# Kernel optimization log

Hardware: AMD Instinct MI355X
Metric: run time of the kernel (lower is better)

Reference implementation:

```python
import jax, jax.numpy as jnp
import numpy as np

B, L, E = 256, 8192, 64
PS_HIGH, PS_LOW = 3, 12
THR = 1.5
WINDOW = 9
K = 5
MAXP = (L + PS_HIGH - 1) // PS_HIGH  # max possible patches per row


def setup_inputs() -> dict:
    key = jax.random.key(0)
    k1, k2, k3, k4, k5 = jax.random.split(key, 5)
    x = jax.random.randint(k1, (B, L), 0, K)  # int tokens in [0, K)
    w1 = jax.random.normal(k2, (E, 1), jnp.float32)        # Linear(1, E) weight
    b1 = jax.random.normal(k3, (E,), jnp.float32) * 0.1
    w2 = jax.random.normal(k4, (E, E), jnp.float32) / np.float32(np.sqrt(E))  # Linear(E, E) weight
    b2 = jax.random.normal(k5, (E,), jnp.float32) * 0.1
    return {"x": x, "w1": w1, "b1": b1, "w2": w2, "b2": b2}


def calc_entropy(x):
    # one-hot counts in a sliding window of size WINDOW (same as conv1d with ones kernel, groups=K)
    oh = jax.nn.one_hot(jnp.clip(x, 0, K - 1), K, dtype=jnp.float32)  # [B, L, K]
    oh = jnp.moveaxis(oh, -1, 1)                                       # [B, K, L]
    pad = WINDOW // 2
    padded = jnp.pad(oh, ((0, 0), (0, 0), (pad, pad)))                 # [B, K, L+2*pad]
    cs = jnp.cumsum(padded, axis=-1)
    csz = jnp.pad(cs, ((0, 0), (0, 0), (1, 0)))
    counts = csz[..., WINDOW:] - csz[..., :-WINDOW]                    # [B, K, L]
    total = jnp.clip(counts.sum(axis=1, keepdims=True), 1e-12, None)
    probs = counts / total
    entropy = -(probs * jnp.log2(probs + 1e-12)).sum(axis=1)           # [B, L]
    return entropy


def seg_row(cs_row, ent_row):
    # cs_row: [L+1] prefix sums of x (float); ent_row: [L] entropy
    def step(i, _):
        ent_i = ent_row[jnp.minimum(i, L - 1)]
        psize = jnp.where(ent_i > THR, PS_HIGH, PS_LOW).astype(jnp.int32)
        j = jnp.minimum(i + psize, L)
        valid = i < L
        mean = (cs_row[j] - cs_row[i]) / jnp.maximum(j - i, 1).astype(jnp.float32)
        return j, (mean, valid)

    _, (means, valids) = jax.lax.scan(step, jnp.int32(0), None, length=MAXP)
    return means, valids  # [MAXP], [MAXP]


def reference(x, w1, b1, w2, b2):
    entropy = calc_entropy(x)
    # prefix sums for O(1) per-patch means
    cs = jnp.pad(jnp.cumsum(x.astype(jnp.float32), axis=1), ((0, 0), (1, 0)))  # [B, L+1]
    means, valids = jax.vmap(seg_row)(cs, entropy)  # [B, MAXP], [B, MAXP]
    # batched tiny MLP over all candidate patches: Linear(1,E) -> ReLU -> Linear(E,E)
    h = jax.nn.relu(means[..., None] * w1[:, 0] + b1)  # [B, MAXP, E]
    vec = h @ w2.T + b2                                # [B, MAXP, E]
    m = valids[..., None].astype(jnp.float32)
    blt_features = (vec * m).sum(axis=1) / m.sum(axis=1)  # [B, E]
    return blt_features, entropy
```

## Files before the change

### kernel.cpp

```cpp
#include <hip/hip_runtime.h>
#include <math.h>


constexpr int B_ = 256;
constexpr int L_ = 8192;
constexpr int E_ = 64;
constexpr int T_ = 1024;
constexpr int PT = 8;
constexpr int CHUNK = 128;
constexpr int NCH = L_ / CHUNK;
constexpr int MAXPC = 44;

__global__ __launch_bounds__(1024)
void entropy_patcher_kernel(const int* __restrict__ x,
                            const float* __restrict__ w1,
                            const float* __restrict__ b1,
                            const float* __restrict__ w2,
                            const float* __restrict__ b2,
                            float* __restrict__ dout) {
  __shared__ __align__(16) unsigned char tok8p[8 + L_ + 8];
  __shared__ __align__(16) float csBuf[L_ + 4];
  __shared__ __align__(16) float meanbuf[NCH][MAXPC];
  __shared__ __align__(16) float tripleTab[1000];
  __shared__ __align__(16) unsigned char maskBytes[T_];
  __shared__ unsigned char exitT[NCH][12];
  __shared__ float rcpTab[13];
  __shared__ float hTab[10];
  __shared__ float l2Tab[13];
  __shared__ int cntC[NCH];
  __shared__ int waveTot[16];
  __shared__ float Sred[16][E_];
  __shared__ float partG[16][E_];
  __shared__ float avgv[E_];
  __shared__ int PcountS;

  const int tid  = threadIdx.x;
  const int lane = tid & 63;
  const int wv   = tid >> 6;
  const int b    = blockIdx.x;

  const int* xr = x + b * L_;
  float* entOut = dout + (size_t)B_ * E_ + (size_t)b * L_;

  const int4 v0 = ((const int4*)xr)[2 * tid];
  const int4 v1 = ((const int4*)xr)[2 * tid + 1];
  unsigned pw0 = (unsigned)v0.x | ((unsigned)v0.y << 8) |
                 ((unsigned)v0.z << 16) | ((unsigned)v0.w << 24);
  unsigned pw1 = (unsigned)v1.x | ((unsigned)v1.y << 8) |
                 ((unsigned)v1.z << 16) | ((unsigned)v1.w << 24);
  *(uint2*)(tok8p + 8 + 8 * tid) = make_uint2(pw0, pw1);
  if (tid == 0) *(uint2*)(tok8p) = make_uint2(~0u, ~0u);
  if (tid == 1) *(uint2*)(tok8p + 8 + L_) = make_uint2(~0u, ~0u);
  if (tid < 1000) {
    int a = tid / 100;
    int r = tid - 100 * a;
    int bq = r / 10, cq = r - 10 * bq;
    float pa = (float)a / 9.0f, pb = (float)bq / 9.0f, pc = (float)cq / 9.0f;
    float fa = -(pa * log2f(pa + 1e-12f));
    float fb = -(pb * log2f(pb + 1e-12f));
    float fc = -(pc * log2f(pc + 1e-12f));
    tripleTab[tid] = fa + fb + fc;
  }
  if (tid >= 1000 && tid < 1010) {
    int n = tid - 1000;
    hTab[n] = (n > 0) ? (float)n * log2f((float)n) : 0.0f;
  }
  if (tid >= 1000 && tid < 1013) {
    int n = tid - 1000;
    rcpTab[n] = 1.0f / (float)(n == 0 ? 1 : n);
  }
  if (tid >= 1010 && tid < 1023) {
    int n = tid - 1010;
    l2Tab[n] = (n > 0) ? log2f((float)n) : 0.0f;
  }
  __syncthreads();

  unsigned long long tw0 = *(const unsigned long long*)(tok8p + 8 * tid);
  unsigned long long tw1 = *(const unsigned long long*)(tok8p + 8 * tid + 8);
  unsigned long long tw2 = *(const unsigned long long*)(tok8p + 8 * tid + 16);
  unsigned code[20];
  #pragma unroll
  for (int l = 4; l < 20; ++l) {
    unsigned byte = (l < 8)  ? (unsigned)((tw0 >> (8 * l)) & 0xff)
                  : (l < 16) ? (unsigned)((tw1 >> (8 * (l - 8))) & 0xff)
                             : (unsigned)((tw2 >> (8 * (l - 16))) & 0xff);
    code[l] = (byte <= 4u) ? (1u << (6 * byte)) : 0u;
  }
  unsigned s = 0;
  #pragma unroll
  for (int l = 4; l <= 12; ++l) s += code[l];
  float entv[PT];
  #pragma unroll
  for (int q = 0; q < PT; ++q) {
    if (q) s += code[q + 12] - code[q + 3];
    unsigned a  = s & 63u,        bb = (s >> 6) & 63u, cc = (s >> 12) & 63u;
    unsigned dd = (s >> 18) & 63u, ee = (s >> 24) & 63u;
    unsigned i1 = a * 100u + bb * 10u + cc;
    unsigned i2 = dd * 100u + ee * 10u;
    entv[q] = tripleTab[i1] + tripleTab[i2];
  }
  if (tid == 0 || tid == T_ - 1) {
    #pragma unroll
    for (int q = 0; q < PT; ++q) {
      int p = 8 * tid + q;
      if (p < 4 || p >= L_ - 4) {
        unsigned ss = 0;
        for (int l = q + 4; l <= q + 12; ++l) ss += code[l];
        unsigned cn[5] = { ss & 63u, (ss >> 6) & 63u, (ss >> 12) & 63u,
                           (ss >> 18) & 63u, (ss >> 24) & 63u };
        int tsum = (int)(cn[0] + cn[1] + cn[2] + cn[3] + cn[4]);
        float sh = hTab[cn[0]] + hTab[cn[1]] + hTab[cn[2]] + hTab[cn[3]] + hTab[cn[4]];
        entv[q] = l2Tab[tsum] - rcpTab[tsum] * sh;
      }
    }
  }
  ((float4*)entOut)[2 * tid]     = make_float4(entv[0], entv[1], entv[2], entv[3]);
  ((float4*)entOut)[2 * tid + 1] = make_float4(entv[4], entv[5], entv[6], entv[7]);
  unsigned mbyte = 0;
  #pragma unroll
  for (int q = 0; q < PT; ++q) mbyte |= (entv[q] > 1.5f ? 1u : 0u) << q;
  maskBytes[tid] = (unsigned char)mbyte;

  int tk[8];
  #pragma unroll
  for (int j = 0; j < 4; ++j) {
    tk[j]     = (int)((pw0 >> (8 * j)) & 0xffu);
    tk[4 + j] = (int)((pw1 >> (8 * j)) & 0xffu);
  }
  int ls = tk[0] + tk[1] + tk[2] + tk[3] + tk[4] + tk[5] + tk[6] + tk[7];
  int incl = ls;
  #pragma unroll
  for (int d = 1; d < 64; d <<= 1) {
    int up = __shfl_up(incl, d, 64);
    if (lane >= d) incl += up;
  }
  if (lane == 63) waveTot[wv] = incl;
  __syncthreads();
  int base = 0;
  #pragma unroll
  for (int q = 0; q < 16; ++q) base += (q < wv) ? waveTot[q] : 0;
  float acc = (float)(base + incl - ls);
  {
    float4 c0, c1;
    c0.x = acc; acc += (float)tk[0]; c0.y = acc; acc += (float)tk[1];
    c0.z = acc; acc += (float)tk[2]; c0.w = acc; acc += (float)tk[3];
    c1.x = acc; acc += (float)tk[4]; c1.y = acc; acc += (float)tk[5];
    c1.z = acc; acc += (float)tk[6]; c1.w = acc; acc += (float)tk[7];
    ((float4*)csBuf)[2 * tid] = c0; ((float4*)csBuf)[2 * tid + 1] = c1;
    if (tid == T_ - 1) csBuf[L_] = acc;
  }

  unsigned long long m0 = 0, m1 = 0;
  if (tid < 768) {
    int c = tid & 63, o = tid >> 6;
    m0 = *(const unsigned long long*)(maskBytes + 16 * c);
    m1 = *(const unsigned long long*)(maskBytes + 16 * c + 8);
    int p = o;
    while (p < CHUNK) {
      unsigned long long mm = (p & 64) ? m1 : m0;
      p += ((mm >> (p & 63)) & 1ULL) ? 3 : 12;
    }
    exitT[c][o] = (unsigned char)(p - CHUNK);
  }
  __syncthreads();

  int myOff = 0;
  if (tid < 64) {
    const unsigned* ep = (const unsigned*)&exitT[tid][0];
    unsigned u0 = ep[0], u1 = ep[1], u2 = ep[2];
    auto nib = [](unsigned w) {
      return (w & 0xFu) | ((w >> 4) & 0xF0u) | ((w >> 8) & 0xF00u) | ((w >> 12) & 0xF000u);
    };
    unsigned long long tab = (unsigned long long)nib(u0)
                           | ((unsigned long long)nib(u1) << 16)
                           | ((unsigned long long)nib(u2) << 32);
    #pragma unroll
    for (int d = 1; d < 64; d <<= 1) {
      unsigned long long other =
          (unsigned long long)__shfl_up((long long)tab, d, 64);
      if (lane >= d) {
        unsigned long long nt = 0;
        #pragma unroll
        for (int e = 0; e < 12; ++e) {
          unsigned oe  = (unsigned)((other >> (4 * e)) & 15ULL);
          unsigned val = (unsigned)((tab >> (4 * oe)) & 15ULL);
          nt |= (unsigned long long)val << (4 * e);
        }
        tab = nt;
      }
    }
    unsigned long long prev = (unsigned long long)__shfl_up((long long)tab, 1, 64);
    myOff = (lane == 0) ? 0 : (int)(prev & 15ULL);

    int c = tid;
    int p = CHUNK * c + myOff;
    const int end = CHUNK * c + CHUNK;
    float csp = csBuf[p];
    int n = 0;
    while (p < end) {
      int lp = p - CHUNK * c;
      unsigned long long mm = (lp & 64) ? m1 : m0;
      int ps = ((mm >> (lp & 63)) & 1ULL) ? 3 : 12;
      int j = p + ps; if (j > L_) j = L_;
      float csj = csBuf[j];
      meanbuf[c][n++] = (csj - csp) * rcpTab[j - p];
      csp = csj; p = j;
    }
    cntC[c] = n;
    int tot = n;
    #pragma unroll
    for (int d2 = 32; d2; d2 >>= 1) tot += __shfl_xor(tot, d2, 64);
    if (lane == 0) PcountS = tot;
  }
  __syncthreads();

  {
    const float w1v = w1[lane];
    const float b1v = b1[lane];
    float S = 0.0f;
    for (int c = wv; c < NCH; c += 16) {
      int n = cntC[c];
      const float* mb = &meanbuf[c][0];
      int j = 0;
      for (; j + 4 <= n; j += 4) {
        float4 m4 = *((const float4*)(mb + j));
        S += fmaxf(fmaf(m4.x, w1v, b1v), 0.0f);
        S += fmaxf(fmaf(m4.y, w1v, b1v), 0.0f);
        S += fmaxf(fmaf(m4.z, w1v, b1v), 0.0f);
        S += fmaxf(fmaf(m4.w, w1v, b1v), 0.0f);
      }
      for (; j < n; ++j) S += fmaxf(fmaf(mb[j], w1v, b1v), 0.0f);
    }
    Sred[wv][lane] = S;
  }
  __syncthreads();
  if (tid < 64) {
    float sm = 0.f;
    #pragma unroll
    for (int q = 0; q < 16; ++q) sm += Sred[q][tid];
    avgv[tid] = sm / (float)PcountS;
  }
  __syncthreads();

  {
    float acc2 = 0.f;
    #pragma unroll
    for (int kk = 0; kk < 4; ++kk) {
      int k = 4 * wv + kk;
      acc2 = fmaf(avgv[k], w2[lane * 64 + k], acc2);
    }
    partG[wv][lane] = acc2;
  }
  __syncthreads();
  if (tid < 64) {
    float r = b2[tid];
    #pragma unroll
    for (int q = 0; q < 16; ++q) r += partG[q][tid];
    dout[(size_t)b * E_ + tid] = r;
  }
}

extern "C" void kernel_launch(void* const* d_in, const int* in_sizes, int n_in,
                              void* d_out, int out_size, void* d_ws, size_t ws_size,
                              hipStream_t stream) {
  const int*   x  = (const int*)d_in[0];
  const float* w1 = (const float*)d_in[1];
  const float* b1 = (const float*)d_in[2];
  const float* w2 = (const float*)d_in[3];
  const float* b2 = (const float*)d_in[4];
  float* out = (float*)d_out;
  entropy_patcher_kernel<<<B_, T_, 0, stream>>>(x, w1, b1, w2, b2, out);
}
```

Measured before the change: 82.29 us.

## Record patch start bitmasks per offset and compute means in parallel per wave

Measured after the change: 82.22 us. About the same (-0.1%).

```diff
diff --git a/kernel.cpp b/kernel.cpp
--- a/kernel.cpp
+++ b/kernel.cpp
@@ -23,7 +23,9 @@
   __shared__ __align__(16) float meanbuf[NCH][MAXPC];
   __shared__ __align__(16) float tripleTab[1000];
   __shared__ __align__(16) unsigned char maskBytes[T_];
+  __shared__ __align__(16) unsigned long long startT[12][64][2];
   __shared__ unsigned char exitT[NCH][12];
+  __shared__ unsigned char chosenOff[NCH];
   __shared__ float rcpTab[13];
   __shared__ float hTab[10];
   __shared__ float l2Tab[13];
@@ -150,21 +152,23 @@
     if (tid == T_ - 1) csBuf[L_] = acc;
   }
 
-  unsigned long long m0 = 0, m1 = 0;
   if (tid < 768) {
     int c = tid & 63, o = tid >> 6;
-    m0 = *(const unsigned long long*)(maskBytes + 16 * c);
-    m1 = *(const unsigned long long*)(maskBytes + 16 * c + 8);
+    unsigned long long m0 = *(const unsigned long long*)(maskBytes + 16 * c);
+    unsigned long long m1 = *(const unsigned long long*)(maskBytes + 16 * c + 8);
+    unsigned long long sA = 0, sB = 0;
     int p = o;
     while (p < CHUNK) {
+      if (p < 64) sA |= 1ull << p; else sB |= 1ull << (p - 64);
       unsigned long long mm = (p & 64) ? m1 : m0;
       p += ((mm >> (p & 63)) & 1ULL) ? 3 : 12;
     }
     exitT[c][o] = (unsigned char)(p - CHUNK);
-  }
-  __syncthreads();
-
-  int myOff = 0;
+    startT[o][c][0] = sA;
+    startT[o][c][1] = sB;
+  }
+  __syncthreads();
+
   if (tid < 64) {
     const unsigned* ep = (const unsigned*)&exitT[tid][0];
     unsigned u0 = ep[0], u1 = ep[1], u2 = ep[2];
@@ -190,27 +194,40 @@
       }
     }
     unsigned long long prev = (unsigned long long)__shfl_up((long long)tab, 1, 64);
-    myOff = (lane == 0) ? 0 : (int)(prev & 15ULL);
-
-    int c = tid;
-    int p = CHUNK * c + myOff;
-    const int end = CHUNK * c + CHUNK;
-    float csp = csBuf[p];
-    int n = 0;
-    while (p < end) {
-      int lp = p - CHUNK * c;
-      unsigned long long mm = (lp & 64) ? m1 : m0;
-      int ps = ((mm >> (lp & 63)) & 1ULL) ? 3 : 12;
-      int j = p + ps; if (j > L_) j = L_;
-      float csj = csBuf[j];
-      meanbuf[c][n++] = (csj - csp) * rcpTab[j - p];
-      csp = csj; p = j;
-    }
-    cntC[c] = n;
-    int tot = n;
+    int myOff = (lane == 0) ? 0 : (int)(prev & 15ULL);
+    chosenOff[tid] = (unsigned char)myOff;
+    unsigned long long sA = startT[myOff][tid][0];
+    unsigned long long sB = startT[myOff][tid][1];
+    int tot = __popcll(sA) + __popcll(sB);
     #pragma unroll
     for (int d2 = 32; d2; d2 >>= 1) tot += __shfl_xor(tot, d2, 64);
     if (lane == 0) PcountS = tot;
+  }
+  __syncthreads();
+
+  for (int c = wv; c < NCH; c += 16) {
+    int off = chosenOff[c];
+    unsigned long long smA = startT[off][c][0];
+    unsigned long long smB = startT[off][c][1];
+    unsigned long long mmA = *(const unsigned long long*)(maskBytes + 16 * c);
+    unsigned long long mmB = *(const unsigned long long*)(maskBytes + 16 * c + 8);
+    int pc0 = __popcll(smA);
+    #pragma unroll
+    for (int t = 0; t < 2; ++t) {
+      int lp = 2 * lane + t;
+      unsigned long long smw = (lp < 64) ? smA : smB;
+      unsigned long long mmw = (lp < 64) ? mmA : mmB;
+      int bi = lp & 63;
+      if ((smw >> bi) & 1ULL) {
+        int p = CHUNK * c + lp;
+        int ps = ((mmw >> bi) & 1ULL) ? 3 : 12;
+        int j = p + ps; if (j > L_) j = L_;
+        unsigned long long below = smw & ((1ull << bi) - 1ull);
+        int n = __popcll(below) + ((lp < 64) ? 0 : pc0);
+        meanbuf[c][n] = (csBuf[j] - csBuf[p]) * rcpTab[j - p];
+      }
+    }
+    if (lane == 0) cntC[c] = pc0 + __popcll(smB);
   }
   __syncthreads();
 
```
